# Kernel tuning notes

Hardware: AMD Instinct MI355X
Metric: run time of the kernel (lower is better)

Reference implementation:

```python
import jax, jax.numpy as jnp
import numpy as np

EMBED = 1024
HEADS = 16
HEAD_DIM = EMBED // HEADS
SCALE = HEAD_DIM ** -0.5


def setup_inputs() -> dict:
    key = jax.random.key(0)
    ks = jax.random.split(key, 5)
    B, N = 2, 2048
    x = jax.random.normal(ks[0], (B, N, EMBED), dtype=jnp.float32)
    # qkv Linear: weight [3*EMBED, EMBED], bias [3*EMBED]
    w_qkv = jax.random.normal(ks[1], (3 * EMBED, EMBED), dtype=jnp.float32) * (EMBED ** -0.5)
    b_qkv = jnp.zeros((3 * EMBED,), dtype=jnp.float32)
    # proj Linear: weight [EMBED, EMBED], bias [EMBED]
    w_proj = jax.random.normal(ks[2], (EMBED, EMBED), dtype=jnp.float32) * (EMBED ** -0.5)
    b_proj = jnp.zeros((EMBED,), dtype=jnp.float32)
    return {"x": x, "w_qkv": w_qkv, "b_qkv": b_qkv, "w_proj": w_proj, "b_proj": b_proj}


def reference(x, w_qkv, b_qkv, w_proj, b_proj):
    B, N, _ = x.shape
    # QKV projection: [B, N, 3*EMBED]
    qkv = jnp.einsum('bnc,dc->bnd', x, w_qkv) + b_qkv
    qkv = qkv.reshape(B, N, 3, HEADS, HEAD_DIM).transpose(2, 0, 3, 1, 4)  # [3, B, H, N, Dh]
    q, k, v = qkv[0], qkv[1], qkv[2]
    # Explicit attention: matmul -> scale -> softmax -> matmul (eval mode, no dropout)
    attn = jnp.einsum('bhqd,bhkd->bhqk', q, k) * SCALE
    attn = jax.nn.softmax(attn, axis=-1)
    out = jnp.einsum('bhqk,bhkd->bhqd', attn, v)
    out = out.transpose(0, 2, 1, 3).reshape(B, N, EMBED)
    # Output projection (gamma1 is Identity; dropouts are zero in eval)
    out = jnp.einsum('bnc,dc->bnd', out, w_proj) + b_proj
    return out
```

## Files before the change

### kernel.cpp

```cpp
#include <hip/hip_runtime.h>
#include <stdint.h>

#define SEQ 2048

typedef __attribute__((ext_vector_type(8))) short bf16x8;
typedef __attribute__((ext_vector_type(4))) float f32x4;
typedef __attribute__((ext_vector_type(4))) int i32x4;

typedef const __attribute__((address_space(1))) unsigned int GVT;
typedef __attribute__((address_space(3))) unsigned int LVT;

static __device__ __forceinline__ unsigned short f2bf(float f) {
  unsigned u = __builtin_bit_cast(unsigned, f);
  u += 0x7fffu + ((u >> 16) & 1u);
  return (unsigned short)(u >> 16);
}

static __device__ __forceinline__ unsigned pk_bf16(float lo, float hi) {
  unsigned r;
  asm("v_cvt_pk_bf16_f32 %0, %1, %2" : "=v"(r) : "v"(lo), "v"(hi));
  return r;
}

__global__ __launch_bounds__(256) void cvt3_kernel(
    const float* __restrict__ s0, unsigned short* __restrict__ d0, int n0,
    const float* __restrict__ s1, unsigned short* __restrict__ d1, int n1,
    const float* __restrict__ s2, unsigned short* __restrict__ d2, int n2) {
  int i = blockIdx.x * 256 + threadIdx.x;
  const int stride = gridDim.x * 256;
  const int total = n0 + n1 + n2;
  for (; i < total; i += stride) {
    const float* s;
    unsigned short* d;
    int k;
    if (i < n0) { s = s0; d = d0; k = i; }
    else if (i < n0 + n1) { s = s1; d = d1; k = i - n0; }
    else { s = s2; d = d2; k = i - n0 - n1; }
    float4 v = reinterpret_cast<const float4*>(s)[k];
    ushort4 o;
    o.x = f2bf(v.x); o.y = f2bf(v.y); o.z = f2bf(v.z); o.w = f2bf(v.w);
    reinterpret_cast<ushort4*>(d)[k] = o;
  }
}

__global__ __launch_bounds__(256, 2) void gemm_qkv_kernel(
    const unsigned short* __restrict__ A,
    const unsigned short* __restrict__ Bt,
    const float* __restrict__ bias,
    unsigned short* __restrict__ qb,
    unsigned short* __restrict__ kbuf,
    unsigned short* __restrict__ vtbuf) {
  __shared__ __align__(16) unsigned short As[2][128 * 32];
  __shared__ __align__(16) unsigned short Bs[2][128 * 32];
  const int tid = threadIdx.x;
  const int lane = tid & 63;
  const int wid = tid >> 6;
  const int wr = wid >> 1, wc = wid & 1;
  const int lin = blockIdx.y * 24 + blockIdx.x;
  const int wg = (lin & 7) * 96 + (lin >> 3);
  const int bm = wg / 24, bn = wg % 24;
  const int lr = lane & 15, hg = lane >> 4;

  f32x4 acc[4][4] = {};

  const int r0 = tid >> 2;
  const int c0 = (tid & 3) * 8;

  auto STAGE = [&](int b, int kt) {
    const unsigned short* ga0 = A + (size_t)(bm * 128 + r0) * 1024 + kt * 32 + c0;
    const unsigned short* ga1 = A + (size_t)(bm * 128 + r0 + 64) * 1024 + kt * 32 + c0;
    const unsigned short* gb0 = Bt + (size_t)(bn * 128 + r0) * 1024 + kt * 32 + c0;
    const unsigned short* gb1 = Bt + (size_t)(bn * 128 + r0 + 64) * 1024 + kt * 32 + c0;
    __builtin_amdgcn_global_load_lds((GVT*)ga0, (LVT*)&As[b][tid * 8], 16, 0, 0);
    __builtin_amdgcn_global_load_lds((GVT*)ga1, (LVT*)&As[b][(tid + 256) * 8], 16, 0, 0);
    __builtin_amdgcn_global_load_lds((GVT*)gb0, (LVT*)&Bs[b][tid * 8], 16, 0, 0);
    __builtin_amdgcn_global_load_lds((GVT*)gb1, (LVT*)&Bs[b][(tid + 256) * 8], 16, 0, 0);
  };

  STAGE(0, 0);
  int cur = 0;
  for (int kt = 0; kt < 32; ++kt) {
    __syncthreads();
    if (kt + 1 < 32) STAGE(cur ^ 1, kt + 1);
    bf16x8 af[4], bfr[4];
#pragma unroll
    for (int i = 0; i < 4; ++i) {
      af[i] = *reinterpret_cast<const bf16x8*>(&As[cur][(wr * 64 + i * 16 + lr) * 32 + hg * 8]);
      bfr[i] = *reinterpret_cast<const bf16x8*>(&Bs[cur][(wc * 64 + i * 16 + lr) * 32 + hg * 8]);
    }
    __builtin_amdgcn_s_setprio(1);
#pragma unroll
    for (int i = 0; i < 4; ++i)
#pragma unroll
      for (int j = 0; j < 4; ++j)
        acc[i][j] = __builtin_amdgcn_mfma_f32_16x16x32_bf16(af[i], bfr[j], acc[i][j], 0, 0, 0);
    __builtin_amdgcn_s_setprio(0);
    cur ^= 1;
  }

#pragma unroll
  for (int j = 0; j < 4; ++j) {
    const int col = bn * 128 + wc * 64 + j * 16 + lr;
    const float bv = bias[col];
    const int which = col >> 10;
    const int hh = (col >> 6) & 15;
    const int dh = col & 63;
    const float scl = which == 0 ? 0.18033688011112042f : 1.0f;
#pragma unroll
    for (int i = 0; i < 4; ++i) {
      if (which == 2) {
        const int row0 = bm * 128 + wr * 64 + i * 16 + hg * 4;
        const int b = row0 >> 11, n0 = row0 & 2047;
        ushort4 vv;
        vv.x = f2bf(acc[i][j][0] + bv);
        vv.y = f2bf(acc[i][j][1] + bv);
        vv.z = f2bf(acc[i][j][2] + bv);
        vv.w = f2bf(acc[i][j][3] + bv);
        *reinterpret_cast<ushort4*>(
            &vtbuf[((size_t)((b * 16 + hh) * 64 + dh)) * 2048 + n0]) = vv;
      } else {
        unsigned short* dst = which == 0 ? qb : kbuf;
#pragma unroll
        for (int r = 0; r < 4; ++r) {
          const int row = bm * 128 + wr * 64 + i * 16 + hg * 4 + r;
          const int b = row >> 11, n = row & 2047;
          dst[((size_t)((b * 16 + hh) * 2048 + n)) * 64 + dh] = f2bf((acc[i][j][r] + bv) * scl);
        }
      }
    }
  }
}

__global__ __launch_bounds__(256, 2) void gemm_proj_kernel(
    const unsigned short* __restrict__ A,
    const unsigned short* __restrict__ Bt,
    const float* __restrict__ bias,
    float* __restrict__ out) {
  __shared__ __align__(16) unsigned short As[2][128 * 32];
  __shared__ __align__(16) unsigned short Bs[2][128 * 32];
  const int tid = threadIdx.x;
  const int lane = tid & 63;
  const int wid = tid >> 6;
  const int wr = wid >> 1, wc = wid & 1;
  const int lin = blockIdx.y * 8 + blockIdx.x;
  const int wg = (lin & 7) * 32 + (lin >> 3);
  const int bm = wg / 8, bn = wg % 8;
  const int lr = lane & 15, hg = lane >> 4;

  f32x4 acc[4][4] = {};
  const int r0 = tid >> 2;
  const int c0 = (tid & 3) * 8;

  auto STAGE = [&](int b, int kt) {
    const unsigned short* ga0 = A + (size_t)(bm * 128 + r0) * 1024 + kt * 32 + c0;
    const unsigned short* ga1 = A + (size_t)(bm * 128 + r0 + 64) * 1024 + kt * 32 + c0;
    const unsigned short* gb0 = Bt + (size_t)(bn * 128 + r0) * 1024 + kt * 32 + c0;
    const unsigned short* gb1 = Bt + (size_t)(bn * 128 + r0 + 64) * 1024 + kt * 32 + c0;
    __builtin_amdgcn_global_load_lds((GVT*)ga0, (LVT*)&As[b][tid * 8], 16, 0, 0);
    __builtin_amdgcn_global_load_lds((GVT*)ga1, (LVT*)&As[b][(tid + 256) * 8], 16, 0, 0);
    __builtin_amdgcn_global_load_lds((GVT*)gb0, (LVT*)&Bs[b][tid * 8], 16, 0, 0);
    __builtin_amdgcn_global_load_lds((GVT*)gb1, (LVT*)&Bs[b][(tid + 256) * 8], 16, 0, 0);
  };

  STAGE(0, 0);
  int cur = 0;
  for (int kt = 0; kt < 32; ++kt) {
    __syncthreads();
    if (kt + 1 < 32) STAGE(cur ^ 1, kt + 1);
    bf16x8 af[4], bfr[4];
#pragma unroll
    for (int i = 0; i < 4; ++i) {
      af[i] = *reinterpret_cast<const bf16x8*>(&As[cur][(wr * 64 + i * 16 + lr) * 32 + hg * 8]);
      bfr[i] = *reinterpret_cast<const bf16x8*>(&Bs[cur][(wc * 64 + i * 16 + lr) * 32 + hg * 8]);
    }
    __builtin_amdgcn_s_setprio(1);
#pragma unroll
    for (int i = 0; i < 4; ++i)
#pragma unroll
      for (int j = 0; j < 4; ++j)
        acc[i][j] = __builtin_amdgcn_mfma_f32_16x16x32_bf16(af[i], bfr[j], acc[i][j], 0, 0, 0);
    __builtin_amdgcn_s_setprio(0);
    cur ^= 1;
  }

#pragma unroll
  for (int j = 0; j < 4; ++j) {
    const int col = bn * 128 + wc * 64 + j * 16 + lr;
    const float bv = bias[col];
#pragma unroll
    for (int i = 0; i < 4; ++i)
#pragma unroll
      for (int r = 0; r < 4; ++r) {
        const int row = bm * 128 + wr * 64 + i * 16 + hg * 4 + r;
        out[(size_t)row * 1024 + col] = acc[i][j][r] + bv;
      }
  }
}

__global__ __launch_bounds__(512, 4) void attn_kernel(
    const unsigned short* __restrict__ qb,
    const unsigned short* __restrict__ kbuf,
    const unsigned short* __restrict__ vt,
    unsigned short* __restrict__ ao) {
  __shared__ __align__(16) unsigned short Ks[2][64 * 64];
  __shared__ __align__(16) unsigned short Vs[2][64 * 64];
  const int tid = threadIdx.x;
  const int lane = tid & 63;
  const int wid = tid >> 6;
  const int lr = lane & 15;
  const int hg = lane >> 4;
  const int lin = blockIdx.y * 16 + blockIdx.x;
  const int wg = (lin & 7) * 64 + (lin >> 3);
  const int qt = wg & 15;
  const int bh = wg >> 4;
  const size_t hbase = (size_t)bh * SEQ * 64;

  bf16x8 qf[2];
  {
    const unsigned short* qp =
        qb + hbase + (size_t)(qt * 128 + wid * 16 + lr) * 64 + hg * 8;
    qf[0] = *reinterpret_cast<const bf16x8*>(qp);
    qf[1] = *reinterpret_cast<const bf16x8*>(qp + 32);
  }

  f32x4 accO[4] = {};
  float m_run = -1e30f;
  float l_run = 0.0f;

  auto STAGE = [&](int b, int kt) {
    const int row = tid >> 3;
    const int sw = ((tid & 7) ^ (row & 7)) * 8;
    const unsigned short* gk = kbuf + hbase + (size_t)(kt * 64 + row) * 64 + sw;
    __builtin_amdgcn_global_load_lds((GVT*)gk, (LVT*)&Ks[b][tid * 8], 16, 0, 0);
    const unsigned short* gv = vt + hbase + (size_t)row * 2048 + kt * 64 + sw;
    __builtin_amdgcn_global_load_lds((GVT*)gv, (LVT*)&Vs[b][tid * 8], 16, 0, 0);
  };

  STAGE(0, 0);
  int cur = 0;
  const int sw0 = (hg ^ (lr & 7)) * 8;
  const int sw1 = ((hg + 4) ^ (lr & 7)) * 8;

  for (int kt = 0; kt < 32; ++kt) {
    __syncthreads();
    if (kt + 1 < 32) STAGE(cur ^ 1, kt + 1);

    f32x4 accT[4] = {};
    __builtin_amdgcn_s_setprio(1);
#pragma unroll
    for (int j = 0; j < 4; ++j) {
      const bf16x8 kf0 = *reinterpret_cast<const bf16x8*>(&Ks[cur][(j * 16 + lr) * 64 + sw0]);
      const bf16x8 kf1 = *reinterpret_cast<const bf16x8*>(&Ks[cur][(j * 16 + lr) * 64 + sw1]);
      accT[j] = __builtin_amdgcn_mfma_f32_16x16x32_bf16(kf0, qf[0], accT[j], 0, 0, 0);
      accT[j] = __builtin_amdgcn_mfma_f32_16x16x32_bf16(kf1, qf[1], accT[j], 0, 0, 0);
    }
    __builtin_amdgcn_s_setprio(0);

    bf16x8 pB[2];
    {
      float t0 = fmaxf(fmaxf(accT[0][0], accT[0][1]), fmaxf(accT[0][2], accT[0][3]));
      float t1 = fmaxf(fmaxf(accT[1][0], accT[1][1]), fmaxf(accT[1][2], accT[1][3]));
      float t2 = fmaxf(fmaxf(accT[2][0], accT[2][1]), fmaxf(accT[2][2], accT[2][3]));
      float t3 = fmaxf(fmaxf(accT[3][0], accT[3][1]), fmaxf(accT[3][2], accT[3][3]));
      float mt = fmaxf(fmaxf(t0, t1), fmaxf(t2, t3));
      mt = fmaxf(mt, __shfl_xor(mt, 16));
      mt = fmaxf(mt, __shfl_xor(mt, 32));
      if (__any(mt > m_run + 8.0f)) {
        const float mnew = fmaxf(m_run, mt);
        const float crr = __builtin_amdgcn_exp2f(m_run - mnew);
        m_run = mnew;
        l_run *= crr;
#pragma unroll
        for (int jd = 0; jd < 4; ++jd)
#pragma unroll
          for (int r = 0; r < 4; ++r) accO[jd][r] *= crr;
      }
      unsigned w[4][2];
      float ps0 = 0.f, ps1 = 0.f;
#pragma unroll
      for (int j = 0; j < 4; ++j) {
        const float p0 = __builtin_amdgcn_exp2f(accT[j][0] - m_run);
        const float p1 = __builtin_amdgcn_exp2f(accT[j][1] - m_run);
        const float p2 = __builtin_amdgcn_exp2f(accT[j][2] - m_run);
        const float p3 = __builtin_amdgcn_exp2f(accT[j][3] - m_run);
        ps0 += (p0 + p1);
        ps1 += (p2 + p3);
        w[j][0] = pk_bf16(p0, p1);
        w[j][1] = pk_bf16(p2, p3);
      }
      float ps = ps0 + ps1;
      ps += __shfl_xor(ps, 16);
      ps += __shfl_xor(ps, 32);
      l_run += ps;
#pragma unroll
      for (int h = 0; h < 2; ++h) {
        unsigned e0 = w[2 * h][0], e1 = w[2 * h][1];
        unsigned f0 = w[2 * h + 1][0], f1 = w[2 * h + 1][1];
        asm("v_permlane32_swap_b32 %0, %1" : "+v"(e0), "+v"(f0));
        asm("v_permlane32_swap_b32 %0, %1" : "+v"(e1), "+v"(f1));
        asm("v_permlane16_swap_b32 %0, %1" : "+v"(e0), "+v"(f0));
        asm("v_permlane16_swap_b32 %0, %1" : "+v"(e1), "+v"(f1));
        const i32x4 pw = {(int)e0, (int)e1, (int)f0, (int)f1};
        pB[h] = __builtin_bit_cast(bf16x8, pw);
      }
    }

    __builtin_amdgcn_s_setprio(1);
#pragma unroll
    for (int jd = 0; jd < 4; ++jd) {
      const bf16x8 v0 = *reinterpret_cast<const bf16x8*>(&Vs[cur][(jd * 16 + lr) * 64 + sw0]);
      const bf16x8 v1 = *reinterpret_cast<const bf16x8*>(&Vs[cur][(jd * 16 + lr) * 64 + sw1]);
      accO[jd] = __builtin_amdgcn_mfma_f32_16x16x32_bf16(v0, pB[0], accO[jd], 0, 0, 0);
      accO[jd] = __builtin_amdgcn_mfma_f32_16x16x32_bf16(v1, pB[1], accO[jd], 0, 0, 0);
    }
    __builtin_amdgcn_s_setprio(0);
    cur ^= 1;
  }

  const int b = bh >> 4, hh = bh & 15;
  {
    const float invl = 1.0f / l_run;
    const int qrow = qt * 128 + wid * 16 + lr;
    unsigned short* dst = ao + (size_t)(b * 2048 + qrow) * 1024 + hh * 64;
#pragma unroll
    for (int jd = 0; jd < 4; ++jd) {
      uint2 o;
      o.x = pk_bf16(accO[jd][0] * invl, accO[jd][1] * invl);
      o.y = pk_bf16(accO[jd][2] * invl, accO[jd][3] * invl);
      *reinterpret_cast<uint2*>(dst + jd * 16 + hg * 4) = o;
    }
  }
}

extern "C" void kernel_launch(void* const* d_in, const int* in_sizes, int n_in,
                              void* d_out, int out_size, void* d_ws, size_t ws_size,
                              hipStream_t stream) {
  const float* x = (const float*)d_in[0];
  const float* w_qkv = (const float*)d_in[1];
  const float* b_qkv = (const float*)d_in[2];
  const float* w_proj = (const float*)d_in[3];
  const float* b_proj = (const float*)d_in[4];
  float* out = (float*)d_out;
  char* ws = (char*)d_ws;
  unsigned short* x_bf = (unsigned short*)(ws);
  unsigned short* ao_bf = (unsigned short*)(ws);
  unsigned short* wq_bf = (unsigned short*)(ws + (8ull << 20));
  unsigned short* wp_bf = (unsigned short*)(ws + (14ull << 20));
  unsigned short* q_bf = (unsigned short*)(ws + (16ull << 20));
  unsigned short* k_bf = (unsigned short*)(ws + (24ull << 20));
  unsigned short* vt_bf = (unsigned short*)(ws + (32ull << 20));

  cvt3_kernel<<<2048, 256, 0, stream>>>(x, x_bf, 4096 * 1024 / 4,
                                        w_qkv, wq_bf, 3072 * 1024 / 4,
                                        w_proj, wp_bf, 1024 * 1024 / 4);
  gemm_qkv_kernel<<<dim3(24, 32), 256, 0, stream>>>(x_bf, wq_bf, b_qkv, q_bf, k_bf, vt_bf);
  attn_kernel<<<dim3(16, 32), 512, 0, stream>>>(q_bf, k_bf, vt_bf, ao_bf);
  gemm_proj_kernel<<<dim3(8, 32), 256, 0, stream>>>(ao_bf, wp_bf, b_proj, out);
}
```

Baseline: 125.6 us.

## Triple-buffer K/V tiles and overlap next QK^T with current softmax-PV

```diff
diff --git a/kernel.cpp b/kernel.cpp
--- a/kernel.cpp
+++ b/kernel.cpp
@@ -202,8 +202,8 @@
     const unsigned short* __restrict__ kbuf,
     const unsigned short* __restrict__ vt,
     unsigned short* __restrict__ ao) {
-  __shared__ __align__(16) unsigned short Ks[2][64 * 64];
-  __shared__ __align__(16) unsigned short Vs[2][64 * 64];
+  __shared__ __align__(16) unsigned short Ks[3 * 64 * 64];
+  __shared__ __align__(16) unsigned short Vs[3 * 64 * 64];
   const int tid = threadIdx.x;
   const int lane = tid & 63;
   const int wid = tid >> 6;
@@ -227,35 +227,36 @@
   float m_run = -1e30f;
   float l_run = 0.0f;
 
-  auto STAGE = [&](int b, int kt) {
-    const int row = tid >> 3;
-    const int sw = ((tid & 7) ^ (row & 7)) * 8;
-    const unsigned short* gk = kbuf + hbase + (size_t)(kt * 64 + row) * 64 + sw;
-    __builtin_amdgcn_global_load_lds((GVT*)gk, (LVT*)&Ks[b][tid * 8], 16, 0, 0);
-    const unsigned short* gv = vt + hbase + (size_t)row * 2048 + kt * 64 + sw;
-    __builtin_amdgcn_global_load_lds((GVT*)gv, (LVT*)&Vs[b][tid * 8], 16, 0, 0);
-  };
-
-  STAGE(0, 0);
-  int cur = 0;
+  const int srow = tid >> 3;
+  const int ssw = ((tid & 7) ^ (srow & 7)) * 8;
+  const unsigned short* kstage0 = kbuf + hbase + (size_t)srow * 64 + ssw;
+  const unsigned short* vstage0 = vt + hbase + (size_t)srow * 2048 + ssw;
+
+  auto STAGE = [&](int kt, int sbuf) {
+    const unsigned short* gk = kstage0 + (size_t)kt * 64 * 64;
+    __builtin_amdgcn_global_load_lds((GVT*)gk, (LVT*)&Ks[sbuf * 4096 + tid * 8], 16, 0, 0);
+    const unsigned short* gv = vstage0 + (size_t)kt * 64;
+    __builtin_amdgcn_global_load_lds((GVT*)gv, (LVT*)&Vs[sbuf * 4096 + tid * 8], 16, 0, 0);
+  };
+
   const int sw0 = (hg ^ (lr & 7)) * 8;
   const int sw1 = ((hg + 4) ^ (lr & 7)) * 8;
 
-  for (int kt = 0; kt < 32; ++kt) {
-    __syncthreads();
-    if (kt + 1 < 32) STAGE(cur ^ 1, kt + 1);
-
-    f32x4 accT[4] = {};
+  auto QKT = [&](int sbuf, f32x4 (&accT)[4]) {
+    const int kb = sbuf * 4096;
     __builtin_amdgcn_s_setprio(1);
 #pragma unroll
     for (int j = 0; j < 4; ++j) {
-      const bf16x8 kf0 = *reinterpret_cast<const bf16x8*>(&Ks[cur][(j * 16 + lr) * 64 + sw0]);
-      const bf16x8 kf1 = *reinterpret_cast<const bf16x8*>(&Ks[cur][(j * 16 + lr) * 64 + sw1]);
-      accT[j] = __builtin_amdgcn_mfma_f32_16x16x32_bf16(kf0, qf[0], accT[j], 0, 0, 0);
-      accT[j] = __builtin_amdgcn_mfma_f32_16x16x32_bf16(kf1, qf[1], accT[j], 0, 0, 0);
+      const bf16x8 kf0 = *reinterpret_cast<const bf16x8*>(&Ks[kb + (j * 16 + lr) * 64 + sw0]);
+      const bf16x8 kf1 = *reinterpret_cast<const bf16x8*>(&Ks[kb + (j * 16 + lr) * 64 + sw1]);
+      f32x4 z = {};
+      z = __builtin_amdgcn_mfma_f32_16x16x32_bf16(kf0, qf[0], z, 0, 0, 0);
+      accT[j] = __builtin_amdgcn_mfma_f32_16x16x32_bf16(kf1, qf[1], z, 0, 0, 0);
     }
     __builtin_amdgcn_s_setprio(0);
-
+  };
+
+  auto SMPV = [&](int sbuf, f32x4 (&accT)[4]) {
     bf16x8 pB[2];
     {
       float t0 = fmaxf(fmaxf(accT[0][0], accT[0][1]), fmaxf(accT[0][2], accT[0][3]));
@@ -304,17 +305,35 @@
         pB[h] = __builtin_bit_cast(bf16x8, pw);
       }
     }
-
+    const int vb = sbuf * 4096;
     __builtin_amdgcn_s_setprio(1);
 #pragma unroll
     for (int jd = 0; jd < 4; ++jd) {
-      const bf16x8 v0 = *reinterpret_cast<const bf16x8*>(&Vs[cur][(jd * 16 + lr) * 64 + sw0]);
-      const bf16x8 v1 = *reinterpret_cast<const bf16x8*>(&Vs[cur][(jd * 16 + lr) * 64 + sw1]);
+      const bf16x8 v0 = *reinterpret_cast<const bf16x8*>(&Vs[vb + (jd * 16 + lr) * 64 + sw0]);
+      const bf16x8 v1 = *reinterpret_cast<const bf16x8*>(&Vs[vb + (jd * 16 + lr) * 64 + sw1]);
       accO[jd] = __builtin_amdgcn_mfma_f32_16x16x32_bf16(v0, pB[0], accO[jd], 0, 0, 0);
       accO[jd] = __builtin_amdgcn_mfma_f32_16x16x32_bf16(v1, pB[1], accO[jd], 0, 0, 0);
     }
     __builtin_amdgcn_s_setprio(0);
-    cur ^= 1;
+  };
+
+  f32x4 sA[4], sB[4];
+  STAGE(0, 0);
+  STAGE(1, 1);
+  __syncthreads();
+  QKT(0, sA);
+  int s0 = 0, s1 = 1, s2 = 2;
+  for (int kt = 0; kt < 32; kt += 2) {
+    if (kt + 2 < 32) STAGE(kt + 2, s2);
+    QKT(s1, sB);
+    SMPV(s0, sA);
+    __syncthreads();
+    { int t = s0; s0 = s1; s1 = s2; s2 = t; }
+    if (kt + 3 < 32) STAGE(kt + 3, s2);
+    if (kt + 2 < 32) QKT(s1, sA);
+    SMPV(s0, sB);
+    __syncthreads();
+    { int t = s0; s0 = s1; s1 = s2; s2 = t; }
   }
 
   const int b = bh >> 4, hh = bh & 15;
```

Result: no change. 126.2 us (+0.5%).

## Stage 128-key chunks per barrier in attention and raise GEMM occupancy hint

Applied to the files above, without the earlier changes.

```diff
diff --git a/kernel.cpp b/kernel.cpp
--- a/kernel.cpp
+++ b/kernel.cpp
@@ -43,7 +43,7 @@
   }
 }
 
-__global__ __launch_bounds__(256, 2) void gemm_qkv_kernel(
+__global__ __launch_bounds__(256, 3) void gemm_qkv_kernel(
     const unsigned short* __restrict__ A,
     const unsigned short* __restrict__ Bt,
     const float* __restrict__ bias,
@@ -131,7 +131,7 @@
   }
 }
 
-__global__ __launch_bounds__(256, 2) void gemm_proj_kernel(
+__global__ __launch_bounds__(256, 3) void gemm_proj_kernel(
     const unsigned short* __restrict__ A,
     const unsigned short* __restrict__ Bt,
     const float* __restrict__ bias,
@@ -202,8 +202,8 @@
     const unsigned short* __restrict__ kbuf,
     const unsigned short* __restrict__ vt,
     unsigned short* __restrict__ ao) {
-  __shared__ __align__(16) unsigned short Ks[2][64 * 64];
-  __shared__ __align__(16) unsigned short Vs[2][64 * 64];
+  __shared__ __align__(16) unsigned short Ks[2][2][64 * 64];
+  __shared__ __align__(16) unsigned short Vs[2][2][64 * 64];
   const int tid = threadIdx.x;
   const int lane = tid & 63;
   const int wid = tid >> 6;
@@ -227,13 +227,21 @@
   float m_run = -1e30f;
   float l_run = 0.0f;
 
-  auto STAGE = [&](int b, int kt) {
-    const int row = tid >> 3;
-    const int sw = ((tid & 7) ^ (row & 7)) * 8;
-    const unsigned short* gk = kbuf + hbase + (size_t)(kt * 64 + row) * 64 + sw;
-    __builtin_amdgcn_global_load_lds((GVT*)gk, (LVT*)&Ks[b][tid * 8], 16, 0, 0);
-    const unsigned short* gv = vt + hbase + (size_t)row * 2048 + kt * 64 + sw;
-    __builtin_amdgcn_global_load_lds((GVT*)gv, (LVT*)&Vs[b][tid * 8], 16, 0, 0);
+  auto STAGE = [&](int b, int kt2) {
+#pragma unroll
+    for (int c = 0; c < 2; ++c) {
+      const int t = tid + c * 512;
+      const int g = t >> 9;
+      const int u = t & 511;
+      const int row = u >> 3;
+      const int sw = ((u & 7) ^ (row & 7)) * 8;
+      const unsigned short* gk =
+          kbuf + hbase + (size_t)(kt2 * 128 + g * 64 + row) * 64 + sw;
+      __builtin_amdgcn_global_load_lds((GVT*)gk, (LVT*)&Ks[b][g][u * 8], 16, 0, 0);
+      const unsigned short* gv =
+          vt + hbase + (size_t)row * 2048 + kt2 * 128 + g * 64 + sw;
+      __builtin_amdgcn_global_load_lds((GVT*)gv, (LVT*)&Vs[b][g][u * 8], 16, 0, 0);
+    }
   };
 
   STAGE(0, 0);
@@ -241,79 +249,86 @@
   const int sw0 = (hg ^ (lr & 7)) * 8;
   const int sw1 = ((hg + 4) ^ (lr & 7)) * 8;
 
-  for (int kt = 0; kt < 32; ++kt) {
+  for (int kt2 = 0; kt2 < 16; ++kt2) {
     __syncthreads();
-    if (kt + 1 < 32) STAGE(cur ^ 1, kt + 1);
-
-    f32x4 accT[4] = {};
-    __builtin_amdgcn_s_setprio(1);
-#pragma unroll
-    for (int j = 0; j < 4; ++j) {
-      const bf16x8 kf0 = *reinterpret_cast<const bf16x8*>(&Ks[cur][(j * 16 + lr) * 64 + sw0]);
-      const bf16x8 kf1 = *reinterpret_cast<const bf16x8*>(&Ks[cur][(j * 16 + lr) * 64 + sw1]);
-      accT[j] = __builtin_amdgcn_mfma_f32_16x16x32_bf16(kf0, qf[0], accT[j], 0, 0, 0);
-      accT[j] = __builtin_amdgcn_mfma_f32_16x16x32_bf16(kf1, qf[1], accT[j], 0, 0, 0);
-    }
-    __builtin_amdgcn_s_setprio(0);
-
-    bf16x8 pB[2];
-    {
-      float t0 = fmaxf(fmaxf(accT[0][0], accT[0][1]), fmaxf(accT[0][2], accT[0][3]));
-      float t1 = fmaxf(fmaxf(accT[1][0], accT[1][1]), fmaxf(accT[1][2], accT[1][3]));
-      float t2 = fmaxf(fmaxf(accT[2][0], accT[2][1]), fmaxf(accT[2][2], accT[2][3]));
-      float t3 = fmaxf(fmaxf(accT[3][0], accT[3][1]), fmaxf(accT[3][2], accT[3][3]));
-      float mt = fmaxf(fmaxf(t0, t1), fmaxf(t2, t3));
-      mt = fmaxf(mt, __shfl_xor(mt, 16));
-      mt = fmaxf(mt, __shfl_xor(mt, 32));
-      if (__any(mt > m_run + 8.0f)) {
-        const float mnew = fmaxf(m_run, mt);
-        const float crr = __builtin_amdgcn_exp2f(m_run - mnew);
-        m_run = mnew;
-        l_run *= crr;
-#pragma unroll
-        for (int jd = 0; jd < 4; ++jd)
-#pragma unroll
-          for (int r = 0; r < 4; ++r) accO[jd][r] *= crr;
-      }
-      unsigned w[4][2];
-      float ps0 = 0.f, ps1 = 0.f;
+    if (kt2 + 1 < 16) STAGE(cur ^ 1, kt2 + 1);
+
+#pragma unroll
+    for (int g = 0; g < 2; ++g) {
+      f32x4 accT[4] = {};
+      __builtin_amdgcn_s_setprio(1);
 #pragma unroll
       for (int j = 0; j < 4; ++j) {
-        const float p0 = __builtin_amdgcn_exp2f(accT[j][0] - m_run);
-        const float p1 = __builtin_amdgcn_exp2f(accT[j][1] - m_run);
-        const float p2 = __builtin_amdgcn_exp2f(accT[j][2] - m_run);
-        const float p3 = __builtin_amdgcn_exp2f(accT[j][3] - m_run);
-        ps0 += (p0 + p1);
-        ps1 += (p2 + p3);
-        w[j][0] = pk_bf16(p0, p1);
-        w[j][1] = pk_bf16(p2, p3);
-      }
-      float ps = ps0 + ps1;
-      ps += __shfl_xor(ps, 16);
-      ps += __shfl_xor(ps, 32);
-      l_run += ps;
-#pragma unroll
-      for (int h = 0; h < 2; ++h) {
-        unsigned e0 = w[2 * h][0], e1 = w[2 * h][1];
-        unsigned f0 = w[2 * h + 1][0], f1 = w[2 * h + 1][1];
-        asm("v_permlane32_swap_b32 %0, %1" : "+v"(e0), "+v"(f0));
-        asm("v_permlane32_swap_b32 %0, %1" : "+v"(e1), "+v"(f1));
-        asm("v_permlane16_swap_b32 %0, %1" : "+v"(e0), "+v"(f0));
-        asm("v_permlane16_swap_b32 %0, %1" : "+v"(e1), "+v"(f1));
-        const i32x4 pw = {(int)e0, (int)e1, (int)f0, (int)f1};
-        pB[h] = __builtin_bit_cast(bf16x8, pw);
-      }
-    }
-
-    __builtin_amdgcn_s_setprio(1);
-#pragma unroll
-    for (int jd = 0; jd < 4; ++jd) {
-      const bf16x8 v0 = *reinterpret_cast<const bf16x8*>(&Vs[cur][(jd * 16 + lr) * 64 + sw0]);
-      const bf16x8 v1 = *reinterpret_cast<const bf16x8*>(&Vs[cur][(jd * 16 + lr) * 64 + sw1]);
-      accO[jd] = __builtin_amdgcn_mfma_f32_16x16x32_bf16(v0, pB[0], accO[jd], 0, 0, 0);
-      accO[jd] = __builtin_amdgcn_mfma_f32_16x16x32_bf16(v1, pB[1], accO[jd], 0, 0, 0);
-    }
-    __builtin_amdgcn_s_setprio(0);
+        const bf16x8 kf0 =
+            *reinterpret_cast<const bf16x8*>(&Ks[cur][g][(j * 16 + lr) * 64 + sw0]);
+        const bf16x8 kf1 =
+            *reinterpret_cast<const bf16x8*>(&Ks[cur][g][(j * 16 + lr) * 64 + sw1]);
+        accT[j] = __builtin_amdgcn_mfma_f32_16x16x32_bf16(kf0, qf[0], accT[j], 0, 0, 0);
+        accT[j] = __builtin_amdgcn_mfma_f32_16x16x32_bf16(kf1, qf[1], accT[j], 0, 0, 0);
+      }
+      __builtin_amdgcn_s_setprio(0);
+
+      bf16x8 pB[2];
+      {
+        float t0 = fmaxf(fmaxf(accT[0][0], accT[0][1]), fmaxf(accT[0][2], accT[0][3]));
+        float t1 = fmaxf(fmaxf(accT[1][0], accT[1][1]), fmaxf(accT[1][2], accT[1][3]));
+        float t2 = fmaxf(fmaxf(accT[2][0], accT[2][1]), fmaxf(accT[2][2], accT[2][3]));
+        float t3 = fmaxf(fmaxf(accT[3][0], accT[3][1]), fmaxf(accT[3][2], accT[3][3]));
+        float mt = fmaxf(fmaxf(t0, t1), fmaxf(t2, t3));
+        mt = fmaxf(mt, __shfl_xor(mt, 16));
+        mt = fmaxf(mt, __shfl_xor(mt, 32));
+        if (__any(mt > m_run + 8.0f)) {
+          const float mnew = fmaxf(m_run, mt);
+          const float crr = __builtin_amdgcn_exp2f(m_run - mnew);
+          m_run = mnew;
+          l_run *= crr;
+#pragma unroll
+          for (int jd = 0; jd < 4; ++jd)
+#pragma unroll
+            for (int r = 0; r < 4; ++r) accO[jd][r] *= crr;
+        }
+        unsigned w[4][2];
+        float ps0 = 0.f, ps1 = 0.f;
+#pragma unroll
+        for (int j = 0; j < 4; ++j) {
+          const float p0 = __builtin_amdgcn_exp2f(accT[j][0] - m_run);
+          const float p1 = __builtin_amdgcn_exp2f(accT[j][1] - m_run);
+          const float p2 = __builtin_amdgcn_exp2f(accT[j][2] - m_run);
+          const float p3 = __builtin_amdgcn_exp2f(accT[j][3] - m_run);
+          ps0 += (p0 + p1);
+          ps1 += (p2 + p3);
+          w[j][0] = pk_bf16(p0, p1);
+          w[j][1] = pk_bf16(p2, p3);
+        }
+        float ps = ps0 + ps1;
+        ps += __shfl_xor(ps, 16);
+        ps += __shfl_xor(ps, 32);
+        l_run += ps;
+#pragma unroll
+        for (int h = 0; h < 2; ++h) {
+          unsigned e0 = w[2 * h][0], e1 = w[2 * h][1];
+          unsigned f0 = w[2 * h + 1][0], f1 = w[2 * h + 1][1];
+          asm("v_permlane32_swap_b32 %0, %1" : "+v"(e0), "+v"(f0));
+          asm("v_permlane32_swap_b32 %0, %1" : "+v"(e1), "+v"(f1));
+          asm("v_permlane16_swap_b32 %0, %1" : "+v"(e0), "+v"(f0));
+          asm("v_permlane16_swap_b32 %0, %1" : "+v"(e1), "+v"(f1));
+          const i32x4 pw = {(int)e0, (int)e1, (int)f0, (int)f1};
+          pB[h] = __builtin_bit_cast(bf16x8, pw);
+        }
+      }
+
+      __builtin_amdgcn_s_setprio(1);
+#pragma unroll
+      for (int jd = 0; jd < 4; ++jd) {
+        const bf16x8 v0 =
+            *reinterpret_cast<const bf16x8*>(&Vs[cur][g][(jd * 16 + lr) * 64 + sw0]);
+        const bf16x8 v1 =
+            *reinterpret_cast<const bf16x8*>(&Vs[cur][g][(jd * 16 + lr) * 64 + sw1]);
+        accO[jd] = __builtin_amdgcn_mfma_f32_16x16x32_bf16(v0, pB[0], accO[jd], 0, 0, 0);
+        accO[jd] = __builtin_amdgcn_mfma_f32_16x16x32_bf16(v1, pB[1], accO[jd], 0, 0, 0);
+      }
+      __builtin_amdgcn_s_setprio(0);
+    }
     cur ^= 1;
   }
 
```

After: 123.5 us. Within noise of the previous version (-1.7%).
